# Kernel optimization log

Hardware: AMD Instinct MI355X
Metric: run time of the kernel (lower is better)

Reference implementation:

```python
import jax, jax.numpy as jnp
import numpy as np

DIM_SINGLE = 384
DIM_PAIR = 128
HEADS = 12
DIM_POINT = 4
B, N = 1, 1024
EPS = 1e-5


def _gram_schmidt_rot(key, shape):
    k1, k2 = jax.random.split(key)
    v1 = jax.random.normal(k1, shape + (3,), jnp.float32)
    v2 = jax.random.normal(k2, shape + (3,), jnp.float32)
    x = v1 / jnp.linalg.norm(v1, axis=-1, keepdims=True)
    z = jnp.cross(x, v2)
    z = z / jnp.linalg.norm(z, axis=-1, keepdims=True)
    y = jnp.cross(z, x)
    # columns are basis vectors, matching torch.stack([x,y,z], dim=-1)
    return jnp.stack([x, y, z], axis=-1)


def setup_inputs() -> dict:
    key = jax.random.key(0)
    ks = jax.random.split(key, 24)
    C, Cp, H, P = DIM_SINGLE, DIM_PAIR, HEADS, DIM_POINT
    HP3 = H * P * 3
    s = lambda k, sh, sc: (jax.random.normal(k, sh, jnp.float32) * sc)
    inp = {
        'single': jax.random.normal(ks[0], (B, N, C), jnp.float32),
        'pair': jax.random.normal(ks[1], (B, N, N, Cp), jnp.float32),
        'rot': _gram_schmidt_rot(ks[2], (B, N)),
        'trans': jax.random.normal(ks[3], (B, N, 3), jnp.float32),
        'mask': jnp.ones((B, N), dtype=bool),
        'Wq': s(ks[4], (C, C), C ** -0.5), 'bq': jnp.zeros((C,), jnp.float32),
        'Wk': s(ks[5], (C, C), C ** -0.5), 'bk': jnp.zeros((C,), jnp.float32),
        'Wv': s(ks[6], (C, C), C ** -0.5), 'bv': jnp.zeros((C,), jnp.float32),
        'Wpb': s(ks[7], (Cp, H), Cp ** -0.5), 'bpb': jnp.zeros((H,), jnp.float32),
        'Wqp': s(ks[8], (C, HP3), C ** -0.5), 'bqp': jnp.zeros((HP3,), jnp.float32),
        'Wkp': s(ks[9], (C, HP3), C ** -0.5), 'bkp': jnp.zeros((HP3,), jnp.float32),
        'Wvp': s(ks[10], (C, HP3), C ** -0.5), 'bvp': jnp.zeros((HP3,), jnp.float32),
        'Wo': s(ks[11], (C, C), C ** -0.5), 'bo': jnp.zeros((C,), jnp.float32),
        'Wpo': s(ks[12], (HP3, C), HP3 ** -0.5), 'bpo': jnp.zeros((C,), jnp.float32),
        'gamma': jnp.ones((C,), jnp.float32), 'beta': jnp.zeros((C,), jnp.float32),
    }
    return inp


def ipa_forward(single, pair, rot, trans, mask,
                Wq, bq, Wk, bk, Wv, bv, Wpb, bpb,
                Wqp, bqp, Wkp, bkp, Wvp, bvp,
                Wo, bo, Wpo, bpo, gamma, beta):
    Bn, Nn, C = single.shape
    H, P = HEADS, DIM_POINT
    Ch = C // H
    scale = Ch ** -0.5

    q = (single @ Wq + bq).reshape(Bn, Nn, H, Ch)
    k = (single @ Wk + bk).reshape(Bn, Nn, H, Ch)
    v = (single @ Wv + bv).reshape(Bn, Nn, H, Ch)

    pair_bias = (pair @ Wpb + bpb).transpose(0, 3, 1, 2)  # [B,H,N,N]

    def pts(W, b):
        p = (single @ W + b).reshape(Bn, Nn, H, P, 3)
        # point as row-vector times rot (matches torch einsum bnhpd,bnhde->bnhpe)
        p = jnp.einsum('bnhpd,bnde->bnhpe', p, rot) + trans[:, :, None, None, :]
        return p

    q_pts = pts(Wqp, bqp)
    k_pts = pts(Wkp, bkp)
    v_pts = pts(Wvp, bvp)

    q2 = jnp.sum(q_pts ** 2, axis=(3, 4))  # [B,N,H]
    k2 = jnp.sum(k_pts ** 2, axis=(3, 4))

    scalar_logits = jnp.einsum('bmhc,bnhc->bhmn', q, k) * scale
    qk_pts = jnp.einsum('bmhpd,bnhpd->bhmn', q_pts, k_pts)
    point_logits = -0.5 * (q2.transpose(0, 2, 1)[:, :, :, None]
                           + k2.transpose(0, 2, 1)[:, :, None, :]
                           - 2.0 * qk_pts) * scale
    logits = scalar_logits + point_logits + pair_bias

    mask2d = mask[:, None, :, None] & mask[:, None, None, :]  # [B,1,M,N]
    logits = jnp.where(mask2d, logits, -1e9)

    attn = jax.nn.softmax(logits, axis=-1)  # [B,H,M,N]

    out_scalar = jnp.einsum('bhmn,bnhc->bmhc', attn, v).reshape(Bn, Nn, C)
    out_points = jnp.einsum('bhmn,bnhpd->bmhpd', attn, v_pts).reshape(Bn, Nn, H * P * 3)

    out = out_scalar @ Wo + bo + out_points @ Wpo + bpo
    x = single + out
    mu = jnp.mean(x, axis=-1, keepdims=True)
    var = jnp.var(x, axis=-1, keepdims=True)
    return (x - mu) / jnp.sqrt(var + EPS) * gamma + beta


def reference(single, pair, rot, trans, mask,
              Wq, bq, Wk, bk, Wv, bv, Wpb, bpb,
              Wqp, bqp, Wkp, bkp, Wvp, bvp,
              Wo, bo, Wpo, bpo, gamma, beta):
    return ipa_forward(single, pair, rot, trans, mask,
                       Wq, bq, Wk, bk, Wv, bv, Wpb, bpb,
                       Wqp, bqp, Wkp, bkp, Wvp, bvp,
                       Wo, bo, Wpo, bpo, gamma, beta)
```

## Files before the change

### kernel.cpp

```cpp
#include <hip/hip_runtime.h>
#include <cmath>


#define SCALE 0.17677669529663687f

#define OFF_QQ 0u
#define OFF_KK 589824u
#define OFF_VV 1179648u
#define OFF_OA 1769472u
#define OFF_LG 2310144u
#define OFF_TMP 14893056u
#define WS_FLOATS 16515072ull

__device__ __forceinline__ void fma4(float4& a, const float4& w, float s) {
  a.x = fmaf(w.x, s, a.x); a.y = fmaf(w.y, s, a.y);
  a.z = fmaf(w.z, s, a.z); a.w = fmaf(w.w, s, a.w);
}

__global__ __launch_bounds__(256) void k_gemm(
    const float* __restrict__ single,
    const float* __restrict__ Wq, const float* __restrict__ bq,
    const float* __restrict__ Wk, const float* __restrict__ bk,
    const float* __restrict__ Wv, const float* __restrict__ bv,
    const float* __restrict__ Wqp, const float* __restrict__ bqp,
    const float* __restrict__ Wkp, const float* __restrict__ bkp,
    const float* __restrict__ Wvp, const float* __restrict__ bvp,
    float* __restrict__ TMP)
{
  __shared__ float sA[64 * 36];
  __shared__ float sB[48 * 36];
  const int tid = threadIdx.x;
  const int m0 = blockIdx.x * 64;
  const int ct = blockIdx.y;
  const float* W; const float* bb; int OUT, cb;
  if (ct < 24) {
    int w_ = ct >> 3;
    W  = w_ == 0 ? Wq : (w_ == 1 ? Wk : Wv);
    bb = w_ == 0 ? bq : (w_ == 1 ? bk : bv);
    OUT = 384; cb = (ct & 7) * 48;
  } else {
    int pt = ct - 24; int w_ = pt / 3;
    W  = w_ == 0 ? Wqp : (w_ == 1 ? Wkp : Wvp);
    bb = w_ == 0 ? bqp : (w_ == 1 ? bkp : bvp);
    OUT = 144; cb = (pt - w_ * 3) * 48;
  }
  const int tr = tid >> 4, tc = tid & 15;
  const int r0 = tr * 4;
  float acc[4][3];
  #pragma unroll
  for (int i = 0; i < 4; ++i)
    #pragma unroll
    for (int j = 0; j < 3; ++j) acc[i][j] = 0.f;

  for (int kc = 0; kc < 12; ++kc) {
    {
      int k4 = tid & 7, mr = tid >> 3;
      *(float4*)&sA[mr * 36 + k4 * 4] =
          *(const float4*)&single[(size_t)(m0 + mr) * 384 + kc * 32 + k4 * 4];
      *(float4*)&sA[(mr + 32) * 36 + k4 * 4] =
          *(const float4*)&single[(size_t)(m0 + mr + 32) * 384 + kc * 32 + k4 * 4];
    }
    for (int f = tid; f < 384; f += 256) {
      int c4 = f % 12, kk = f / 12;
      float4 w = *(const float4*)&W[(size_t)(kc * 32 + kk) * OUT + cb + c4 * 4];
      sB[(c4 * 4 + 0) * 36 + kk] = w.x;
      sB[(c4 * 4 + 1) * 36 + kk] = w.y;
      sB[(c4 * 4 + 2) * 36 + kk] = w.z;
      sB[(c4 * 4 + 3) * 36 + kk] = w.w;
    }
    __syncthreads();
    #pragma unroll
    for (int k4 = 0; k4 < 8; ++k4) {
      float4 av[4], bv_[3];
      #pragma unroll
      for (int i = 0; i < 4; ++i) av[i] = *(const float4*)&sA[(r0 + i) * 36 + k4 * 4];
      #pragma unroll
      for (int j = 0; j < 3; ++j) bv_[j] = *(const float4*)&sB[(tc * 3 + j) * 36 + k4 * 4];
      #pragma unroll
      for (int i = 0; i < 4; ++i)
        #pragma unroll
        for (int j = 0; j < 3; ++j)
          acc[i][j] += av[i].x * bv_[j].x + av[i].y * bv_[j].y
                     + av[i].z * bv_[j].z + av[i].w * bv_[j].w;
    }
    __syncthreads();
  }
  #pragma unroll
  for (int i = 0; i < 4; ++i)
    #pragma unroll
    for (int j = 0; j < 3; ++j) {
      int c = tc * 3 + j;
      TMP[(size_t)(m0 + r0 + i) * 1584 + ct * 48 + c] = acc[i][j] + bb[cb + c];
    }
}

__global__ __launch_bounds__(256) void k_epi(
    const float* __restrict__ TMP, const float* __restrict__ rotm,
    const float* __restrict__ trans, const float* __restrict__ bpb,
    float* __restrict__ ws)
{
  __shared__ float srot[288];
  const int tid = threadIdx.x;
  const int m = blockIdx.x;
  const float* t = TMP + (size_t)m * 1584;
  float* QQ = ws + OFF_QQ; float* KK = ws + OFF_KK; float* VV = ws + OFF_VV;

  for (int i = tid; i < 1152; i += 256) {
    int seg = i / 384, idx = i - seg * 384;
    int h = idx >> 5, c = idx & 31;
    float val = t[i];
    if (seg == 0)      QQ[h * 49152 + m * 48 + c] = SCALE * val;
    else if (seg == 1) KK[h * 49152 + m * 48 + c] = val;
    else               VV[m * 576 + h * 48 + c] = val;
  }
  const float* R = rotm + m * 9;
  for (int i = tid; i < 432; i += 256) {
    int seg = i / 144, r = i - seg * 144;
    int h = r / 12, pe = r - h * 12, p = pe / 3, e = pe - p * 3;
    const float* raw = t + 1152 + seg * 144 + h * 12 + p * 3;
    float val = raw[0] * R[e] + raw[1] * R[3 + e] + raw[2] * R[6 + e] + trans[m * 3 + e];
    if (seg == 0)      { srot[r] = val;       QQ[h * 49152 + m * 48 + 32 + pe] = SCALE * val; }
    else if (seg == 1) { srot[144 + r] = val; KK[h * 49152 + m * 48 + 32 + pe] = val; }
    else               VV[m * 576 + h * 48 + 32 + pe] = val;
  }
  __syncthreads();
  if (tid < 24) {
    int seg = tid / 12, h = tid - seg * 12;
    float s2 = 0.f;
    #pragma unroll
    for (int j = 0; j < 12; ++j) {
      float x = srot[seg * 144 + h * 12 + j];
      s2 = fmaf(x, x, s2);
    }
    if (seg == 0) {
      float* d = QQ + h * 49152 + m * 48;
      d[44] = 1.f; d[45] = -0.5f * SCALE * s2; d[46] = 0.f; d[47] = 0.f;
    } else {
      float* d = KK + h * 49152 + m * 48;
      d[44] = bpb[h] - 0.5f * SCALE * s2; d[45] = 1.f; d[46] = 0.f; d[47] = 0.f;
    }
  }
}

__global__ __launch_bounds__(256) void k_qkdot(const float* __restrict__ QQ,
                                               const float* __restrict__ KK,
                                               float* __restrict__ LG)
{
  __shared__ float sQ[64 * 52];
  __shared__ float sK[128 * 52];
  const int tid = threadIdx.x;
  const int n0 = blockIdx.x * 128, m0 = blockIdx.y * 64, hh = blockIdx.z;
  const float* Qg = QQ + (size_t)hh * 49152 + (size_t)m0 * 48;
  const float* Kg = KK + (size_t)hh * 49152 + (size_t)n0 * 48;
  for (int i = tid; i < 768; i += 256) {
    int r = i / 12, c4 = (i - r * 12) * 4;
    *(float4*)&sQ[r * 52 + c4] = *(const float4*)&Qg[r * 48 + c4];
  }
  for (int i = tid; i < 1536; i += 256) {
    int r = i / 12, c4 = (i - r * 12) * 4;
    *(float4*)&sK[r * 52 + c4] = *(const float4*)&Kg[r * 48 + c4];
  }
  __syncthreads();
  const int mb = (tid >> 4) * 4, nb = tid & 15;
  float acc[4][8];
  #pragma unroll
  for (int i = 0; i < 4; ++i)
    #pragma unroll
    for (int j = 0; j < 8; ++j) acc[i][j] = 0.f;
  #pragma unroll
  for (int j4 = 0; j4 < 48; j4 += 4) {
    float4 q[4], k[8];
    #pragma unroll
    for (int i = 0; i < 4; ++i) q[i] = *(const float4*)&sQ[(mb + i) * 52 + j4];
    #pragma unroll
    for (int j = 0; j < 8; ++j) k[j] = *(const float4*)&sK[(nb + j * 16) * 52 + j4];
    #pragma unroll
    for (int i = 0; i < 4; ++i)
      #pragma unroll
      for (int j = 0; j < 8; ++j)
        acc[i][j] += q[i].x * k[j].x + q[i].y * k[j].y + q[i].z * k[j].z + q[i].w * k[j].w;
  }
  float* Lb = LG + (size_t)hh * 1048576 + (size_t)m0 * 1024 + n0;
  #pragma unroll
  for (int i = 0; i < 4; ++i)
    #pragma unroll
    for (int j = 0; j < 8; ++j)
      Lb[(mb + i) * 1024 + nb + j * 16] = acc[i][j];
}

__global__ __launch_bounds__(256) void k_bias(const float* __restrict__ pair,
                                              const float* __restrict__ Wpb,
                                              float* __restrict__ LG)
{
  __shared__ float sP[256 * 33];
  const int tid = threadIdx.x;
  const size_t base = (size_t)blockIdx.x * 256;
  const int c4 = tid & 7, r8 = tid >> 3;
  float acc[12];
  #pragma unroll
  for (int h = 0; h < 12; ++h) acc[h] = 0.f;

  float4 pre[8];
  #pragma unroll
  for (int k = 0; k < 8; ++k)
    pre[k] = *(const float4*)&pair[(base + k * 32 + r8) * 128 + c4 * 4];

  for (int cc = 0; cc < 4; ++cc) {
    #pragma unroll
    for (int k = 0; k < 8; ++k) {
      float* d = &sP[(k * 32 + r8) * 33 + c4 * 4];
      d[0] = pre[k].x; d[1] = pre[k].y; d[2] = pre[k].z; d[3] = pre[k].w;
    }
    if (cc < 3) {
      #pragma unroll
      for (int k = 0; k < 8; ++k)
        pre[k] = *(const float4*)&pair[(base + k * 32 + r8) * 128 + (cc + 1) * 32 + c4 * 4];
    }
    __syncthreads();
    const float* rp = &sP[tid * 33];
    #pragma unroll 8
    for (int j = 0; j < 32; ++j) {
      float p = rp[j];
      const float* w = Wpb + (cc * 32 + j) * 12;
      #pragma unroll
      for (int h = 0; h < 12; ++h) acc[h] = fmaf(p, w[h], acc[h]);
    }
    __syncthreads();
  }
  float* L = LG + base + tid;
  #pragma unroll
  for (int h = 0; h < 12; ++h) L[(size_t)h * 1048576] += acc[h];
}

__global__ __launch_bounds__(256) void k_smax_av(const float* __restrict__ LG,
                                                 const float* __restrict__ VV,
                                                 float* __restrict__ OA)
{
  __shared__ float sW[16 * 268];
  __shared__ float sM[16];
  __shared__ float sL[16];
  __shared__ float sF[16];
  const int tid = threadIdx.x;
  const int hh = blockIdx.y, m0 = blockIdx.x * 16;
  const int lane = tid & 63, wv = tid >> 6;
  const float* Lh = LG + (size_t)hh * 1048576;
  if (tid < 16) { sM[tid] = -3.0e38f; sL[tid] = 0.f; }
  __syncthreads();

  const int mi = tid & 15, cg = tid >> 4;
  float4 a1 = make_float4(0.f, 0.f, 0.f, 0.f);
  const float* vbase = VV + hh * 48;

  for (int nc = 0; nc < 1024; nc += 256) {
    #pragma unroll
    for (int rr = 0; rr < 4; ++rr) {
      int r = wv * 4 + rr;
      float4 x = *(const float4*)&Lh[(size_t)(m0 + r) * 1024 + nc + lane * 4];
      float mx = fmaxf(fmaxf(x.x, x.y), fmaxf(x.z, x.w));
      #pragma unroll
      for (int s = 32; s; s >>= 1) mx = fmaxf(mx, __shfl_xor(mx, s));
      float mo = sM[r];
      float mn = fmaxf(mo, mx);
      float4 e;
      e.x = __expf(x.x - mn); e.y = __expf(x.y - mn);
      e.z = __expf(x.z - mn); e.w = __expf(x.w - mn);
      float sum = e.x + e.y + e.z + e.w;
      #pragma unroll
      for (int s = 32; s; s >>= 1) sum += __shfl_xor(sum, s);
      if (lane == 0) {
        float f = __expf(mo - mn);
        sF[r] = f; sM[r] = mn; sL[r] = sL[r] * f + sum;
      }
      *(float4*)&sW[r * 268 + lane * 4] = e;
    }
    __syncthreads();
    float f = sF[mi];
    a1.x *= f; a1.y *= f; a1.z *= f; a1.w *= f;
    if (cg < 11) {
      #pragma unroll 4
      for (int nn4 = 0; nn4 < 64; ++nn4) {
        float4 p = *(const float4*)&sW[mi * 268 + nn4 * 4];
        const float* vr = vbase + (size_t)(nc + nn4 * 4) * 576 + cg * 4;
        float4 w0 = *(const float4*)(vr);
        float4 w1 = *(const float4*)(vr + 576);
        float4 w2 = *(const float4*)(vr + 1152);
        float4 w3 = *(const float4*)(vr + 1728);
        fma4(a1, w0, p.x); fma4(a1, w1, p.y); fma4(a1, w2, p.z); fma4(a1, w3, p.w);
      }
    }
    __syncthreads();
  }
  if (cg < 11) {
    float is = 1.f / sL[mi];
    float* o1 = OA + (size_t)(m0 + mi) * 528 + hh * 44 + cg * 4;
    o1[0] = a1.x * is; o1[1] = a1.y * is; o1[2] = a1.z * is; o1[3] = a1.w * is;
  }
}

__global__ __launch_bounds__(128) void k_final(
    const float* __restrict__ OA, const float* __restrict__ single,
    const float* __restrict__ Wo, const float* __restrict__ bo,
    const float* __restrict__ Wpo, const float* __restrict__ bpo,
    const float* __restrict__ gamma, const float* __restrict__ beta,
    float* __restrict__ out)
{
  __shared__ float sX[2 * 384];
  const int tid = threadIdx.x;
  const int m0 = blockIdx.x * 2;
  if (tid < 96) {
    int o4 = tid * 4;
    float4 b1 = *(const float4*)&bo[o4];
    float4 b2 = *(const float4*)&bpo[o4];
    float4 bs = make_float4(b1.x + b2.x, b1.y + b2.y, b1.z + b2.z, b1.w + b2.w);
    float4 acc[2] = {bs, bs};
    const float* oab = OA + (size_t)m0 * 528;
    #pragma unroll 1
    for (int hh = 0; hh < 12; ++hh) {
      #pragma unroll
      for (int j4 = 0; j4 < 8; ++j4) {
        const float* wp = Wo + (size_t)(hh * 32 + j4 * 4) * 384 + o4;
        float4 w0 = *(const float4*)(wp);
        float4 w1 = *(const float4*)(wp + 384);
        float4 w2 = *(const float4*)(wp + 768);
        float4 w3 = *(const float4*)(wp + 1152);
        #pragma unroll
        for (int mi = 0; mi < 2; ++mi) {
          float4 s = *(const float4*)(oab + mi * 528 + hh * 44 + j4 * 4);
          fma4(acc[mi], w0, s.x); fma4(acc[mi], w1, s.y);
          fma4(acc[mi], w2, s.z); fma4(acc[mi], w3, s.w);
        }
      }
      #pragma unroll
      for (int j4 = 0; j4 < 3; ++j4) {
        const float* wp = Wpo + (size_t)(hh * 12 + j4 * 4) * 384 + o4;
        float4 w0 = *(const float4*)(wp);
        float4 w1 = *(const float4*)(wp + 384);
        float4 w2 = *(const float4*)(wp + 768);
        float4 w3 = *(const float4*)(wp + 1152);
        #pragma unroll
        for (int mi = 0; mi < 2; ++mi) {
          float4 s = *(const float4*)(oab + mi * 528 + hh * 44 + 32 + j4 * 4);
          fma4(acc[mi], w0, s.x); fma4(acc[mi], w1, s.y);
          fma4(acc[mi], w2, s.z); fma4(acc[mi], w3, s.w);
        }
      }
    }
    #pragma unroll
    for (int mi = 0; mi < 2; ++mi) {
      float4 sg = *(const float4*)&single[(size_t)(m0 + mi) * 384 + o4];
      float4 x = make_float4(acc[mi].x + sg.x, acc[mi].y + sg.y,
                             acc[mi].z + sg.z, acc[mi].w + sg.w);
      *(float4*)&sX[mi * 384 + o4] = x;
    }
  }
  __syncthreads();
  const int lane = tid & 63, r = tid >> 6;
  float xs[6]; float s = 0.f;
  #pragma unroll
  for (int i = 0; i < 6; ++i) { xs[i] = sX[r * 384 + lane * 6 + i]; s += xs[i]; }
  #pragma unroll
  for (int d = 32; d; d >>= 1) s += __shfl_xor(s, d);
  float mu = s * (1.f / 384.f);
  float vs = 0.f;
  #pragma unroll
  for (int i = 0; i < 6; ++i) { float dd = xs[i] - mu; vs = fmaf(dd, dd, vs); }
  #pragma unroll
  for (int d = 32; d; d >>= 1) vs += __shfl_xor(vs, d);
  float rstd = rsqrtf(vs * (1.f / 384.f) + 1e-5f);
  #pragma unroll
  for (int i = 0; i < 6; ++i) {
    int c = lane * 6 + i;
    out[(size_t)(m0 + r) * 384 + c] = (xs[i] - mu) * rstd * gamma[c] + beta[c];
  }
}

__global__ void k_wsfail(float* out, int n) {
  int i = blockIdx.x * 256 + threadIdx.x;
  if (i < n) out[i] = 12345.0f;
}

extern "C" void kernel_launch(void* const* d_in, const int* in_sizes, int n_in,
                              void* d_out, int out_size, void* d_ws, size_t ws_size,
                              hipStream_t stream)
{
  (void)in_sizes; (void)n_in;
  const float* single = (const float*)d_in[0];
  const float* pair   = (const float*)d_in[1];
  const float* rotm   = (const float*)d_in[2];
  const float* trans  = (const float*)d_in[3];
  const float* Wq  = (const float*)d_in[5];
  const float* bq  = (const float*)d_in[6];
  const float* Wk  = (const float*)d_in[7];
  const float* bk  = (const float*)d_in[8];
  const float* Wv  = (const float*)d_in[9];
  const float* bv  = (const float*)d_in[10];
  const float* Wpb = (const float*)d_in[11];
  const float* bpb = (const float*)d_in[12];
  const float* Wqp = (const float*)d_in[13];
  const float* bqp = (const float*)d_in[14];
  const float* Wkp = (const float*)d_in[15];
  const float* bkp = (const float*)d_in[16];
  const float* Wvp = (const float*)d_in[17];
  const float* bvp = (const float*)d_in[18];
  const float* Wo  = (const float*)d_in[19];
  const float* bo  = (const float*)d_in[20];
  const float* Wpo = (const float*)d_in[21];
  const float* bpo = (const float*)d_in[22];
  const float* gamma = (const float*)d_in[23];
  const float* beta  = (const float*)d_in[24];
  float* ws  = (float*)d_ws;
  float* out = (float*)d_out;

  if (ws_size < WS_FLOATS * 4ull) {
    k_wsfail<<<(out_size + 255) / 256, 256, 0, stream>>>(out, out_size);
    return;
  }

  k_gemm<<<dim3(16, 33), 256, 0, stream>>>(single,
      Wq, bq, Wk, bk, Wv, bv, Wqp, bqp, Wkp, bkp, Wvp, bvp, ws + OFF_TMP);
  k_epi<<<1024, 256, 0, stream>>>(ws + OFF_TMP, rotm, trans, bpb, ws);
  k_qkdot<<<dim3(8, 16, 12), 256, 0, stream>>>(ws + OFF_QQ, ws + OFF_KK, ws + OFF_LG);
  k_bias<<<4096, 256, 0, stream>>>(pair, Wpb, ws + OFF_LG);
  k_smax_av<<<dim3(64, 12), 256, 0, stream>>>(ws + OFF_LG, ws + OFF_VV, ws + OFF_OA);
  k_final<<<512, 128, 0, stream>>>(ws + OFF_OA, single, Wo, bo, Wpo, bpo,
                                   gamma, beta, out);
}
```

Measured before the change: 349.8 us.

## Fuse QK point/scalar dot into pair-bias kernel to avoid logits round trip

Removes the separate QK dot-product kernel and computes each logit's Q·K term inside the pair-bias kernel before adding the bias projection. The logits buffer is then written once instead of being written and later read-modify-written. In exchange, each thread reads its K row per head from global memory with strided access instead of using a shared-memory tiled GEMM, so performance relies on L2 reuse of K.

```diff
diff --git a/kernel.cpp b/kernel.cpp
--- a/kernel.cpp
+++ b/kernel.cpp
@@ -142,68 +142,43 @@
   }
 }
 
-__global__ __launch_bounds__(256) void k_qkdot(const float* __restrict__ QQ,
-                                               const float* __restrict__ KK,
-                                               float* __restrict__ LG)
-{
-  __shared__ float sQ[64 * 52];
-  __shared__ float sK[128 * 52];
-  const int tid = threadIdx.x;
-  const int n0 = blockIdx.x * 128, m0 = blockIdx.y * 64, hh = blockIdx.z;
-  const float* Qg = QQ + (size_t)hh * 49152 + (size_t)m0 * 48;
-  const float* Kg = KK + (size_t)hh * 49152 + (size_t)n0 * 48;
-  for (int i = tid; i < 768; i += 256) {
-    int r = i / 12, c4 = (i - r * 12) * 4;
-    *(float4*)&sQ[r * 52 + c4] = *(const float4*)&Qg[r * 48 + c4];
-  }
-  for (int i = tid; i < 1536; i += 256) {
-    int r = i / 12, c4 = (i - r * 12) * 4;
-    *(float4*)&sK[r * 52 + c4] = *(const float4*)&Kg[r * 48 + c4];
-  }
-  __syncthreads();
-  const int mb = (tid >> 4) * 4, nb = tid & 15;
-  float acc[4][8];
-  #pragma unroll
-  for (int i = 0; i < 4; ++i)
-    #pragma unroll
-    for (int j = 0; j < 8; ++j) acc[i][j] = 0.f;
-  #pragma unroll
-  for (int j4 = 0; j4 < 48; j4 += 4) {
-    float4 q[4], k[8];
-    #pragma unroll
-    for (int i = 0; i < 4; ++i) q[i] = *(const float4*)&sQ[(mb + i) * 52 + j4];
-    #pragma unroll
-    for (int j = 0; j < 8; ++j) k[j] = *(const float4*)&sK[(nb + j * 16) * 52 + j4];
-    #pragma unroll
-    for (int i = 0; i < 4; ++i)
-      #pragma unroll
-      for (int j = 0; j < 8; ++j)
-        acc[i][j] += q[i].x * k[j].x + q[i].y * k[j].y + q[i].z * k[j].z + q[i].w * k[j].w;
-  }
-  float* Lb = LG + (size_t)hh * 1048576 + (size_t)m0 * 1024 + n0;
-  #pragma unroll
-  for (int i = 0; i < 4; ++i)
-    #pragma unroll
-    for (int j = 0; j < 8; ++j)
-      Lb[(mb + i) * 1024 + nb + j * 16] = acc[i][j];
-}
-
-__global__ __launch_bounds__(256) void k_bias(const float* __restrict__ pair,
-                                              const float* __restrict__ Wpb,
-                                              float* __restrict__ LG)
+__global__ __launch_bounds__(256) void k_biasdot(const float* __restrict__ pair,
+                                                 const float* __restrict__ Wpb,
+                                                 const float* __restrict__ QQ,
+                                                 const float* __restrict__ KK,
+                                                 float* __restrict__ LG)
 {
   __shared__ float sP[256 * 33];
+  __shared__ float sQ[576];
   const int tid = threadIdx.x;
   const size_t base = (size_t)blockIdx.x * 256;
+  const int m = blockIdx.x >> 2;
+  const int n = ((blockIdx.x & 3) << 8) | tid;
   const int c4 = tid & 7, r8 = tid >> 3;
-  float acc[12];
-  #pragma unroll
-  for (int h = 0; h < 12; ++h) acc[h] = 0.f;
-
+
+  if (tid < 144) {
+    int h = tid / 12, q4 = (tid - h * 12) * 4;
+    *(float4*)&sQ[h * 48 + q4] = *(const float4*)&QQ[h * 49152 + m * 48 + q4];
+  }
   float4 pre[8];
   #pragma unroll
   for (int k = 0; k < 8; ++k)
     pre[k] = *(const float4*)&pair[(base + k * 32 + r8) * 128 + c4 * 4];
+  __syncthreads();
+
+  float acc[12];
+  #pragma unroll
+  for (int h = 0; h < 12; ++h) {
+    const float* kp = &KK[h * 49152 + n * 48];
+    float a = 0.f;
+    #pragma unroll
+    for (int j4 = 0; j4 < 12; ++j4) {
+      float4 kv = *(const float4*)&kp[j4 * 4];
+      float4 qv = *(const float4*)&sQ[h * 48 + j4 * 4];
+      a += kv.x * qv.x + kv.y * qv.y + kv.z * qv.z + kv.w * qv.w;
+    }
+    acc[h] = a;
+  }
 
   for (int cc = 0; cc < 4; ++cc) {
     #pragma unroll
@@ -229,7 +204,7 @@
   }
   float* L = LG + base + tid;
   #pragma unroll
-  for (int h = 0; h < 12; ++h) L[(size_t)h * 1048576] += acc[h];
+  for (int h = 0; h < 12; ++h) L[(size_t)h * 1048576] = acc[h];
 }
 
 __global__ __launch_bounds__(256) void k_smax_av(const float* __restrict__ LG,
@@ -419,8 +394,8 @@
   k_gemm<<<dim3(16, 33), 256, 0, stream>>>(single,
       Wq, bq, Wk, bk, Wv, bv, Wqp, bqp, Wkp, bkp, Wvp, bvp, ws + OFF_TMP);
   k_epi<<<1024, 256, 0, stream>>>(ws + OFF_TMP, rotm, trans, bpb, ws);
-  k_qkdot<<<dim3(8, 16, 12), 256, 0, stream>>>(ws + OFF_QQ, ws + OFF_KK, ws + OFF_LG);
-  k_bias<<<4096, 256, 0, stream>>>(pair, Wpb, ws + OFF_LG);
+  k_biasdot<<<4096, 256, 0, stream>>>(pair, Wpb, ws + OFF_QQ, ws + OFF_KK,
+                                      ws + OFF_LG);
   k_smax_av<<<dim3(64, 12), 256, 0, stream>>>(ws + OFF_LG, ws + OFF_VV, ws + OFF_OA);
   k_final<<<512, 128, 0, stream>>>(ws + OFF_OA, single, Wo, bo, Wpo, bpo,
                                    gamma, beta, out);
```

After: 642.1 us. +83.6%, slower.

## Double-buffer logits chunks in softmax-AV and retile pair-bias loads

Applied to the files above, without the earlier changes.

The pair-bias kernel now processes the pair channels in 16-wide chunks. It prefetches two chunks ahead, stages them with float4 stores into a narrower padded shared tile, and reads that tile as float4 in the inner FMA loop. The softmax-AV kernel splits each row into 128-wide chunks and prefetches the next chunk's logits into registers while the current chunk is consumed. It also double-buffers the probability and rescale arrays in shared memory, which removes one barrier per chunk. These changes aim to hide global-load latency and cut synchronization. The cost is more loop iterations with more frequent online-softmax rescaling. There is also a risk of register pressure or scratch spills from the runtime-indexed prefetch arrays.

```diff
diff --git a/kernel.cpp b/kernel.cpp
--- a/kernel.cpp
+++ b/kernel.cpp
@@ -192,38 +192,51 @@
                                               const float* __restrict__ Wpb,
                                               float* __restrict__ LG)
 {
-  __shared__ float sP[256 * 33];
+  __shared__ float sP[256 * 17];
   const int tid = threadIdx.x;
   const size_t base = (size_t)blockIdx.x * 256;
-  const int c4 = tid & 7, r8 = tid >> 3;
   float acc[12];
   #pragma unroll
   for (int h = 0; h < 12; ++h) acc[h] = 0.f;
 
-  float4 pre[8];
-  #pragma unroll
-  for (int k = 0; k < 8; ++k)
-    pre[k] = *(const float4*)&pair[(base + k * 32 + r8) * 128 + c4 * 4];
-
-  for (int cc = 0; cc < 4; ++cc) {
-    #pragma unroll
-    for (int k = 0; k < 8; ++k) {
-      float* d = &sP[(k * 32 + r8) * 33 + c4 * 4];
-      d[0] = pre[k].x; d[1] = pre[k].y; d[2] = pre[k].z; d[3] = pre[k].w;
-    }
-    if (cc < 3) {
-      #pragma unroll
-      for (int k = 0; k < 8; ++k)
-        pre[k] = *(const float4*)&pair[(base + k * 32 + r8) * 128 + (cc + 1) * 32 + c4 * 4];
+  float4 pre[2][4];
+  #pragma unroll
+  for (int k = 0; k < 4; ++k) {
+    int fi = tid + k * 256;
+    pre[0][k] = *(const float4*)&pair[(base + (fi >> 2)) * 128 + 0 * 16 + (fi & 3) * 4];
+  }
+  #pragma unroll
+  for (int k = 0; k < 4; ++k) {
+    int fi = tid + k * 256;
+    pre[1][k] = *(const float4*)&pair[(base + (fi >> 2)) * 128 + 1 * 16 + (fi & 3) * 4];
+  }
+
+  for (int cc = 0; cc < 8; ++cc) {
+    const int pb = cc & 1;
+    #pragma unroll
+    for (int k = 0; k < 4; ++k) {
+      int fi = tid + k * 256;
+      *(float4*)&sP[(fi >> 2) * 17 + (fi & 3) * 4] = pre[pb][k];
+    }
+    if (cc < 6) {
+      #pragma unroll
+      for (int k = 0; k < 4; ++k) {
+        int fi = tid + k * 256;
+        pre[pb][k] = *(const float4*)&pair[(base + (fi >> 2)) * 128 + (cc + 2) * 16 + (fi & 3) * 4];
+      }
     }
     __syncthreads();
-    const float* rp = &sP[tid * 33];
-    #pragma unroll 8
-    for (int j = 0; j < 32; ++j) {
-      float p = rp[j];
-      const float* w = Wpb + (cc * 32 + j) * 12;
-      #pragma unroll
-      for (int h = 0; h < 12; ++h) acc[h] = fmaf(p, w[h], acc[h]);
+    const float* rp = &sP[tid * 17];
+    #pragma unroll
+    for (int j4 = 0; j4 < 4; ++j4) {
+      float4 p = *(const float4*)&rp[j4 * 4];
+      const float* w = Wpb + (cc * 16 + j4 * 4) * 12;
+      #pragma unroll
+      for (int h = 0; h < 12; ++h)
+        acc[h] = fmaf(p.x, w[h],
+                 fmaf(p.y, w[12 + h],
+                 fmaf(p.z, w[24 + h],
+                 fmaf(p.w, w[36 + h], acc[h]))));
     }
     __syncthreads();
   }
@@ -236,10 +249,10 @@
                                                  const float* __restrict__ VV,
                                                  float* __restrict__ OA)
 {
-  __shared__ float sW[16 * 268];
+  __shared__ float sW[2][16 * 132];
+  __shared__ float sF[2][16];
   __shared__ float sM[16];
   __shared__ float sL[16];
-  __shared__ float sF[16];
   const int tid = threadIdx.x;
   const int hh = blockIdx.y, m0 = blockIdx.x * 16;
   const int lane = tid & 63, wv = tid >> 6;
@@ -251,36 +264,47 @@
   float4 a1 = make_float4(0.f, 0.f, 0.f, 0.f);
   const float* vbase = VV + hh * 48;
 
-  for (int nc = 0; nc < 1024; nc += 256) {
+  float2 cur[4];
+  #pragma unroll
+  for (int rr = 0; rr < 4; ++rr)
+    cur[rr] = *(const float2*)&Lh[(size_t)(m0 + wv * 4 + rr) * 1024 + lane * 2];
+
+  for (int c = 0; c < 8; ++c) {
+    const int buf = c & 1;
+    float2 nxt[4];
+    if (c < 7) {
+      #pragma unroll
+      for (int rr = 0; rr < 4; ++rr)
+        nxt[rr] = *(const float2*)&Lh[(size_t)(m0 + wv * 4 + rr) * 1024 + (c + 1) * 128 + lane * 2];
+    }
     #pragma unroll
     for (int rr = 0; rr < 4; ++rr) {
       int r = wv * 4 + rr;
-      float4 x = *(const float4*)&Lh[(size_t)(m0 + r) * 1024 + nc + lane * 4];
-      float mx = fmaxf(fmaxf(x.x, x.y), fmaxf(x.z, x.w));
+      float2 x = cur[rr];
+      float mx = fmaxf(x.x, x.y);
       #pragma unroll
       for (int s = 32; s; s >>= 1) mx = fmaxf(mx, __shfl_xor(mx, s));
       float mo = sM[r];
       float mn = fmaxf(mo, mx);
-      float4 e;
-      e.x = __expf(x.x - mn); e.y = __expf(x.y - mn);
-      e.z = __expf(x.z - mn); e.w = __expf(x.w - mn);
-      float sum = e.x + e.y + e.z + e.w;
+      float ex = __expf(x.x - mn), ey = __expf(x.y - mn);
+      float sum = ex + ey;
       #pragma unroll
       for (int s = 32; s; s >>= 1) sum += __shfl_xor(sum, s);
       if (lane == 0) {
         float f = __expf(mo - mn);
-        sF[r] = f; sM[r] = mn; sL[r] = sL[r] * f + sum;
+        sF[buf][r] = f; sM[r] = mn; sL[r] = sL[r] * f + sum;
       }
-      *(float4*)&sW[r * 268 + lane * 4] = e;
+      sW[buf][r * 132 + lane * 2]     = ex;
+      sW[buf][r * 132 + lane * 2 + 1] = ey;
     }
     __syncthreads();
-    float f = sF[mi];
+    float f = sF[buf][mi];
     a1.x *= f; a1.y *= f; a1.z *= f; a1.w *= f;
     if (cg < 11) {
       #pragma unroll 4
-      for (int nn4 = 0; nn4 < 64; ++nn4) {
-        float4 p = *(const float4*)&sW[mi * 268 + nn4 * 4];
-        const float* vr = vbase + (size_t)(nc + nn4 * 4) * 576 + cg * 4;
+      for (int nn4 = 0; nn4 < 32; ++nn4) {
+        float4 p = *(const float4*)&sW[buf][mi * 132 + nn4 * 4];
+        const float* vr = vbase + (size_t)(c * 128 + nn4 * 4) * 576 + cg * 4;
         float4 w0 = *(const float4*)(vr);
         float4 w1 = *(const float4*)(vr + 576);
         float4 w2 = *(const float4*)(vr + 1152);
@@ -288,7 +312,8 @@
         fma4(a1, w0, p.x); fma4(a1, w1, p.y); fma4(a1, w2, p.z); fma4(a1, w3, p.w);
       }
     }
-    __syncthreads();
+    #pragma unroll
+    for (int rr = 0; rr < 4; ++rr) cur[rr] = nxt[rr];
   }
   if (cg < 11) {
     float is = 1.f / sL[mi];
```

Measured after the change: 515.5 us. +47.4%, slower.
